# Optimization experiments

Measured on AMD Instinct MI355X. Metric: run time of the kernel, lower is better.

The kernel has to match this reference:

```python
import jax, jax.numpy as jnp
import numpy as np

VOCAB, EMB, HID, LAT = 32000, 512, 1024, 512
B, T = 32, 128


def setup_inputs() -> dict:
    key = jax.random.key(0)
    ks = jax.random.split(key, 10)
    s = 0.02
    return {
        "latent_vector": jax.random.normal(ks[0], (B, LAT), jnp.float32),
        "target_tokens": jax.random.randint(ks[1], (B, T), 0, VOCAB),
        "emb": jax.random.normal(ks[2], (VOCAB, EMB), jnp.float32) * s,
        "W_lh": jax.random.normal(ks[3], (HID, LAT), jnp.float32) * s,
        "b_lh": jnp.zeros((HID,), jnp.float32),
        "W_ih": jax.random.normal(ks[4], (4 * HID, EMB), jnp.float32) * s,
        "b_ih": jnp.zeros((4 * HID,), jnp.float32),
        "W_hh": jax.random.normal(ks[5], (4 * HID, HID), jnp.float32) * s,
        "b_hh": jnp.zeros((4 * HID,), jnp.float32),
        "W_out": jax.random.normal(ks[6], (VOCAB, HID), jnp.float32) * s,
        "b_out": jnp.zeros((VOCAB,), jnp.float32),
    }


def reference(latent_vector, target_tokens, emb, W_lh, b_lh, W_ih, b_ih, W_hh, b_hh, W_out, b_out):
    # teacher_forcing_ratio = 1.0 (deterministic): input at step t is target_tokens[:, t-1]
    h = latent_vector @ W_lh.T + b_lh            # [B, HID]
    c = jnp.zeros_like(h)
    xs = emb[target_tokens[:, :-1]]              # [B, T-1, EMB]
    xs = jnp.swapaxes(xs, 0, 1)                  # [T-1, B, EMB]

    def step(carry, x):
        h, c = carry
        gates = x @ W_ih.T + b_ih + h @ W_hh.T + b_hh   # [B, 4*HID]
        i, f, g, o = jnp.split(gates, 4, axis=-1)       # PyTorch LSTM gate order
        c = jax.nn.sigmoid(f) * c + jax.nn.sigmoid(i) * jnp.tanh(g)
        h = jax.nn.sigmoid(o) * jnp.tanh(c)
        logits = h @ W_out.T + b_out                    # [B, VOCAB]
        return (h, c), logits

    _, logits = jax.lax.scan(step, (h, c), xs)          # [T-1, B, VOCAB]
    return jnp.swapaxes(logits, 0, 1)                   # [B, T-1, VOCAB]
```

## Files before the change

### kernel.cpp

```cpp
#include <hip/hip_runtime.h>
#include <cstdint>

typedef __bf16 bf16x8 __attribute__((ext_vector_type(8)));
typedef __bf16 bf16x4 __attribute__((ext_vector_type(4)));
typedef float  f32x4  __attribute__((ext_vector_type(4)));

#define VOCAB 32000
#define EMB   512
#define HID   1024
#define LAT   512
#define BATCH 32
#define TSTEP 127
#define MROWS 4064
#define MPAD  4096
#define G4    4096
#define NBLK  128
#define NTM   32
#define NTN   250
#define FSTRIDE 64

__device__ __forceinline__ float sigf(float x){ return 1.0f / (1.0f + __expf(-x)); }
__device__ __forceinline__ float tanhfast(float x){
    float ax = fabsf(x);
    float e  = __expf(-2.0f * ax);
    float t  = (1.0f - e) / (1.0f + e);
    return copysignf(t, x);
}

__device__ __forceinline__ void gll16(void* lds, const void* gsrc){
    __builtin_amdgcn_global_load_lds(
        (const __attribute__((address_space(1))) unsigned int*)gsrc,
        (__attribute__((address_space(3))) unsigned int*)lds,
        16, 0, 0);
}
__device__ __forceinline__ void bar(){ asm volatile("s_barrier" ::: "memory"); }

__global__ __launch_bounds__(256) void init_kernel(
    const float* __restrict__ latent,
    const float* __restrict__ Wlh,
    const float* __restrict__ blh,
    __bf16* __restrict__ h0,
    __bf16* __restrict__ Hall,
    unsigned* __restrict__ flags,
    const float* __restrict__ Whh,
    __bf16* __restrict__ Whhb)
{
    if (blockIdx.x >= 128){
        const int n4 = G4 * HID / 4;
        for (int i = (blockIdx.x - 128) * 256 + threadIdx.x; i < n4; i += 64 * 256){
            float4 v = ((const float4*)Whh)[i];
            bf16x4 o = { (__bf16)v.x, (__bf16)v.y, (__bf16)v.z, (__bf16)v.w };
            ((bf16x4*)Whhb)[i] = o;
        }
        return;
    }
    if (blockIdx.x == 0 && threadIdx.x < NBLK)
        flags[threadIdx.x * FSTRIDE] = 0u;

    int id = blockIdx.x * 256 + threadIdx.x;
    int b = id >> 10, j = id & 1023;
    float s = blh[j];
    const float4* lr = (const float4*)(latent + (size_t)b * LAT);
    const float4* wr = (const float4*)(Wlh + (size_t)j * LAT);
    for (int k = 0; k < LAT / 4; ++k){
        float4 a = lr[k], w = wr[k];
        s += a.x * w.x + a.y * w.y + a.z * w.z + a.w * w.w;
    }
    h0[id] = (__bf16)s;
    Hall[(size_t)MROWS * HID + id] = (__bf16)0.0f;
}

__global__ __launch_bounds__(256) void gemm_xg(
    const float* __restrict__ emb,
    const float* __restrict__ Wih,
    const int*   __restrict__ tok,
    float*       __restrict__ xg,
    const float* __restrict__ bih,
    const float* __restrict__ bhh)
{
    __shared__ __bf16 As[2][128 * 32];
    __shared__ __bf16 Bs[2][128 * 32];

    const int tid  = threadIdx.x;
    const int wid  = tid >> 6, lane = tid & 63;
    const int tile_n = blockIdx.x, tile_m = blockIdx.y;
    const int wr = wid >> 1, wc = wid & 1;

    f32x4 acc[4][4] = {};

    auto stage = [&](int kt, int buf){
        #pragma unroll
        for (int j = 0; j < 2; ++j){
            const int slot = tid + j * 256;
            const int row  = slot >> 2;
            const int kb   = kt * 32 + (slot & 3) * 8;
            {
                const int brow = tile_n * 128 + row;
                const float4* p = (const float4*)(Wih + (size_t)brow * EMB + kb);
                float4 u = p[0], v = p[1];
                bf16x8 w = { (__bf16)u.x, (__bf16)u.y, (__bf16)u.z, (__bf16)u.w,
                             (__bf16)v.x, (__bf16)v.y, (__bf16)v.z, (__bf16)v.w };
                *(bf16x8*)&Bs[buf][row * 32 + (slot & 3) * 8] = w;
            }
            {
                int r = tile_m * 128 + row;
                int rc = (r < MROWS) ? r : (MROWS - 1);
                int token = tok[(rc & 31) * 128 + (rc >> 5)];
                const float4* p = (const float4*)(emb + (size_t)token * EMB + kb);
                float4 u = p[0], v = p[1];
                bf16x8 w = { (__bf16)u.x, (__bf16)u.y, (__bf16)u.z, (__bf16)u.w,
                             (__bf16)v.x, (__bf16)v.y, (__bf16)v.z, (__bf16)v.w };
                *(bf16x8*)&As[buf][row * 32 + (slot & 3) * 8] = w;
            }
        }
    };

    const int KT = EMB / 32;
    stage(0, 0);
    for (int kt = 0; kt < KT; ++kt){
        const int buf = kt & 1;
        __syncthreads();
        if (kt + 1 < KT) stage(kt + 1, buf ^ 1);
        const __bf16* Abuf = As[buf];
        const __bf16* Bbuf = Bs[buf];
        const int ar = lane & 15, ko = (lane >> 4) * 8;
        bf16x8 av[4], bv[4];
        #pragma unroll
        for (int m = 0; m < 4; ++m)
            av[m] = *(const bf16x8*)&Abuf[(wr * 64 + m * 16 + ar) * 32 + ko];
        #pragma unroll
        for (int n = 0; n < 4; ++n)
            bv[n] = *(const bf16x8*)&Bbuf[(wc * 64 + n * 16 + ar) * 32 + ko];
        #pragma unroll
        for (int m = 0; m < 4; ++m)
            #pragma unroll
            for (int n = 0; n < 4; ++n)
                acc[m][n] = __builtin_amdgcn_mfma_f32_16x16x32_bf16(av[m], bv[n], acc[m][n], 0, 0, 0);
    }

    const int r0 = tile_m * 128 + wr * 64 + ((lane >> 4) << 2);
    const int c0 = tile_n * 128 + wc * 64 + (lane & 15);
    #pragma unroll
    for (int m = 0; m < 4; ++m){
        #pragma unroll
        for (int n = 0; n < 4; ++n){
            const int col = c0 + n * 16;
            float badd = bih[col] + bhh[col];
            #pragma unroll
            for (int q = 0; q < 4; ++q){
                int row = r0 + m * 16 + q;
                xg[(size_t)row * G4 + col] = acc[m][n][q] + badd;
            }
        }
    }
}

__global__ __launch_bounds__(512) void gemm_logits8(
    const __bf16* __restrict__ A,
    const __bf16* __restrict__ B,
    float*        __restrict__ C,
    const float*  __restrict__ bias)
{
    __shared__ __bf16 sA[4][256][32];
    __shared__ __bf16 sB[4][256][32];

    const int tid = threadIdx.x;
    const int wid = tid >> 6, lane = tid & 63;
    const int wm = wid >> 2, wn = wid & 3;

    const int bid = blockIdx.x;
    const int s   = (bid & 7) * 250 + (bid >> 3);
    const int g   = s / 500, rem = s % 500;
    const int tm  = g * 4 + (rem & 3);
    const int tn  = rem >> 2;

    const int sr  = tid >> 2;
    const int scb = tid & 3;
    const __bf16* gA = A + (size_t)(tm * 256 + sr) * HID + scb * 8;
    const __bf16* gB = B + (size_t)(tn * 256 + sr) * HID + scb * 8;
    char* const dA0 = (char*)&sA[0][0][0] + wid * 1024;
    char* const dB0 = (char*)&sB[0][0][0] + wid * 1024;

    auto stageA = [&](int kt){
        const int sl = kt & 3;
        gll16(dA0 + sl * 16384,        gA + (size_t)kt * 32);
        gll16(dA0 + sl * 16384 + 8192, gA + (size_t)128 * HID + (size_t)kt * 32);
    };
    auto stageB = [&](int kt){
        const int sl = kt & 3;
        gll16(dB0 + sl * 16384,        gB + (size_t)kt * 32);
        gll16(dB0 + sl * 16384 + 8192, gB + (size_t)128 * HID + (size_t)kt * 32);
    };

    f32x4 acc[8][4] = {};
    const int fr = lane & 15, fk = (lane >> 4) * 8;

    stageA(0); stageB(0); stageA(1); stageB(1); stageA(2); stageB(2);
    asm volatile("s_waitcnt vmcnt(8)" ::: "memory");
    bar();

    const int KT = HID / 32;
    bf16x8 bfr[4], afr[4];
    for (int kt = 0; kt < KT; ++kt){
        const int sl = kt & 3;
        #pragma unroll
        for (int nf = 0; nf < 4; ++nf)
            bfr[nf] = *(const bf16x8*)&sB[sl][wn * 64 + nf * 16 + fr][fk];
        #pragma unroll
        for (int mf = 0; mf < 4; ++mf)
            afr[mf] = *(const bf16x8*)&sA[sl][wm * 128 + mf * 16 + fr][fk];
        if (kt + 3 < KT) stageA(kt + 3);
        bar();
        asm volatile("s_waitcnt lgkmcnt(0)" ::: "memory");
        __builtin_amdgcn_sched_barrier(0);
        __builtin_amdgcn_s_setprio(1);
        #pragma unroll
        for (int mf = 0; mf < 4; ++mf)
            #pragma unroll
            for (int nf = 0; nf < 4; ++nf)
                acc[mf][nf] = __builtin_amdgcn_mfma_f32_16x16x32_bf16(
                    afr[mf], bfr[nf], acc[mf][nf], 0, 0, 0);
        __builtin_amdgcn_s_setprio(0);
        bar();
        #pragma unroll
        for (int mf = 0; mf < 4; ++mf)
            afr[mf] = *(const bf16x8*)&sA[sl][wm * 128 + (mf + 4) * 16 + fr][fk];
        if (kt + 3 < KT) stageB(kt + 3);
        bar();
        asm volatile("s_waitcnt lgkmcnt(0)" ::: "memory");
        __builtin_amdgcn_sched_barrier(0);
        __builtin_amdgcn_s_setprio(1);
        #pragma unroll
        for (int mf = 0; mf < 4; ++mf)
            #pragma unroll
            for (int nf = 0; nf < 4; ++nf)
                acc[mf + 4][nf] = __builtin_amdgcn_mfma_f32_16x16x32_bf16(
                    afr[mf], bfr[nf], acc[mf + 4][nf], 0, 0, 0);
        __builtin_amdgcn_s_setprio(0);
        if (kt < KT - 3)       asm volatile("s_waitcnt vmcnt(8)" ::: "memory");
        else if (kt == KT - 3) asm volatile("s_waitcnt vmcnt(4)" ::: "memory");
        else if (kt == KT - 2) asm volatile("s_waitcnt vmcnt(0)" ::: "memory");
        bar();
    }

    #pragma unroll
    for (int mf = 0; mf < 8; ++mf){
        #pragma unroll
        for (int nf = 0; nf < 4; ++nf){
            const int col = tn * 256 + wn * 64 + nf * 16 + fr;
            const float badd = bias[col];
            #pragma unroll
            for (int q = 0; q < 4; ++q){
                int row = tm * 256 + wm * 128 + mf * 16 + (lane >> 4) * 4 + q;
                if (row < MROWS){
                    int t = row >> 5, b = row & 31;
                    __builtin_nontemporal_store(acc[mf][nf][q] + badd,
                        &C[((size_t)b * TSTEP + t) * VOCAB + col]);
                }
            }
        }
    }
}

template<int BF16B>
__global__ __launch_bounds__(256) void gemm_logits(
    const __bf16* __restrict__ A,
    const float*  __restrict__ Bf,
    const __bf16* __restrict__ Bb,
    float*        __restrict__ C,
    const float*  __restrict__ bias)
{
    __shared__ __bf16 As[2][128 * 32];
    __shared__ __bf16 Bs[2][128 * 32];

    const int tid  = threadIdx.x;
    const int wid  = tid >> 6, lane = tid & 63;
    const int bid = blockIdx.x;
    const int s   = (bid & 7) * (NTM * NTN / 8) + (bid >> 3);
    const int g   = s / (8 * NTN), rem = s % (8 * NTN);
    const int tile_m = g * 8 + (rem & 7);
    const int tile_n = rem >> 3;
    const int wr = wid >> 1, wc = wid & 1;

    f32x4 acc[4][4] = {};

    auto stage = [&](int kt, int buf){
        const int kb = kt * 32 + (lane & 3) * 8;
        #pragma unroll
        for (int c2 = 0; c2 < 2; ++c2){
            int rA = tile_m * 128 + c2 * 64 + wid * 16 + (lane >> 2);
            gll16(&As[buf][c2 * 2048 + wid * 512], A + (size_t)rA * HID + kb);
            if constexpr (BF16B){
                int rB = tile_n * 128 + c2 * 64 + wid * 16 + (lane >> 2);
                gll16(&Bs[buf][c2 * 2048 + wid * 512], Bb + (size_t)rB * HID + kb);
            }
        }
        if constexpr (!BF16B){
            #pragma unroll
            for (int j = 0; j < 2; ++j){
                const int slot = tid + j * 256;
                const int row  = slot >> 2;
                const int kb2  = kt * 32 + (slot & 3) * 8;
                const int brow = tile_n * 128 + row;
                const float4* p = (const float4*)(Bf + (size_t)brow * HID + kb2);
                float4 u = p[0], v = p[1];
                bf16x8 w = { (__bf16)u.x, (__bf16)u.y, (__bf16)u.z, (__bf16)u.w,
                             (__bf16)v.x, (__bf16)v.y, (__bf16)v.z, (__bf16)v.w };
                *(bf16x8*)&Bs[buf][row * 32 + (slot & 3) * 8] = w;
            }
        }
    };

    const int KT = HID / 32;
    stage(0, 0);
    for (int kt = 0; kt < KT; ++kt){
        const int buf = kt & 1;
        __syncthreads();
        if (kt + 1 < KT) stage(kt + 1, buf ^ 1);
        const __bf16* Abuf = As[buf];
        const __bf16* Bbuf = Bs[buf];
        const int ar = lane & 15, ko = (lane >> 4) * 8;
        bf16x8 av[4], bv[4];
        #pragma unroll
        for (int m = 0; m < 4; ++m)
            av[m] = *(const bf16x8*)&Abuf[(wr * 64 + m * 16 + ar) * 32 + ko];
        #pragma unroll
        for (int n = 0; n < 4; ++n)
            bv[n] = *(const bf16x8*)&Bbuf[(wc * 64 + n * 16 + ar) * 32 + ko];
        #pragma unroll
        for (int m = 0; m < 4; ++m)
            #pragma unroll
            for (int n = 0; n < 4; ++n)
                acc[m][n] = __builtin_amdgcn_mfma_f32_16x16x32_bf16(av[m], bv[n], acc[m][n], 0, 0, 0);
    }

    const int r0 = tile_m * 128 + wr * 64 + ((lane >> 4) << 2);
    const int c0 = tile_n * 128 + wc * 64 + (lane & 15);
    #pragma unroll
    for (int m = 0; m < 4; ++m){
        #pragma unroll
        for (int n = 0; n < 4; ++n){
            const int col = c0 + n * 16;
            float badd = bias[col];
            #pragma unroll
            for (int q = 0; q < 4; ++q){
                int row = r0 + m * 16 + q;
                if (row < MROWS){
                    int t = row >> 5, b = row & 31;
                    __builtin_nontemporal_store(acc[m][n][q] + badd,
                        &C[((size_t)b * TSTEP + t) * VOCAB + col]);
                }
            }
        }
    }
}

__global__ __launch_bounds__(256) void lstm_coop(
    const float*  __restrict__ xg,
    __bf16*       __restrict__ Hall,
    __bf16*       __restrict__ hbuf,
    const __bf16* __restrict__ Whhb,
    unsigned*     __restrict__ flags,
    const float*  __restrict__ Woutf,
    __bf16*       __restrict__ Woutb)
{
    if (blockIdx.x >= NBLK){
        if (Woutb){
            const int n4 = VOCAB * HID / 4;
            for (int i = (blockIdx.x - NBLK) * 256 + threadIdx.x; i < n4; i += NBLK * 256){
                float4 v = ((const float4*)Woutf)[i];
                bf16x4 o = { (__bf16)v.x, (__bf16)v.y, (__bf16)v.z, (__bf16)v.w };
                ((bf16x4*)Woutb)[i] = o;
            }
        }
        return;
    }

    __shared__ float lds_g[4 * 4 * 4 * 64];
    const int tid = threadIdx.x, wid = tid >> 6, lane = tid & 63;
    const int jb = blockIdx.x * 8;

    bf16x8 bfrag[2][8];
    {
        const int gl = lane & 15, ko = (lane >> 4) * 8;
        #pragma unroll
        for (int nt = 0; nt < 2; ++nt){
            int gg = nt * 16 + gl;
            const __bf16* base =
                Whhb + (size_t)((gg >> 3) * HID + jb + (gg & 7)) * HID + wid * 256 + ko;
            #pragma unroll
            for (int ks = 0; ks < 8; ++ks)
                bfrag[nt][ks] = *(const bf16x8*)(base + ks * 32);
        }
    }

    const int b2 = tid >> 2, up0 = (tid & 3) * 2;
    const int mt2 = b2 >> 4, r2 = b2 & 15, reg2 = r2 & 3, lb2 = (r2 >> 2) << 4;
    float cst[2] = {0.0f, 0.0f};

    const float* xq = xg + (size_t)b2 * G4 + jb + up0;
    float2 xv[4];
    if (tid < 128){
        #pragma unroll
        for (int g = 0; g < 4; ++g) xv[g] = *(const float2*)(xq + g * HID);
    }

    const size_t e0 = (size_t)(lane & 15) * HID + wid * 256 + (lane >> 4) * 8;

    for (int t = 0; t < TSTEP; ++t){
        const unsigned long long* hq =
            (const unsigned long long*)(hbuf + (size_t)(t & 1) * (BATCH * HID));
        union { unsigned long long q[2]; bf16x8 v; } xa[16];
        #pragma unroll
        for (int ks = 0; ks < 8; ++ks){
            size_t q0 = (e0 + (size_t)ks * 32) >> 2;
            size_t q1 = q0 + ((size_t)16 * HID >> 2);
            xa[ks].q[0]     = __hip_atomic_load(hq + q0,     __ATOMIC_RELAXED, __HIP_MEMORY_SCOPE_AGENT);
            xa[ks].q[1]     = __hip_atomic_load(hq + q0 + 1, __ATOMIC_RELAXED, __HIP_MEMORY_SCOPE_AGENT);
            xa[8 + ks].q[0] = __hip_atomic_load(hq + q1,     __ATOMIC_RELAXED, __HIP_MEMORY_SCOPE_AGENT);
            xa[8 + ks].q[1] = __hip_atomic_load(hq + q1 + 1, __ATOMIC_RELAXED, __HIP_MEMORY_SCOPE_AGENT);
        }
        f32x4 a00 = {}, a01 = {}, a10 = {}, a11 = {};
        #pragma unroll
        for (int ks = 0; ks < 8; ++ks){
            a00 = __builtin_amdgcn_mfma_f32_16x16x32_bf16(xa[ks].v,     bfrag[0][ks], a00, 0, 0, 0);
            a01 = __builtin_amdgcn_mfma_f32_16x16x32_bf16(xa[ks].v,     bfrag[1][ks], a01, 0, 0, 0);
            a10 = __builtin_amdgcn_mfma_f32_16x16x32_bf16(xa[8 + ks].v, bfrag[0][ks], a10, 0, 0, 0);
            a11 = __builtin_amdgcn_mfma_f32_16x16x32_bf16(xa[8 + ks].v, bfrag[1][ks], a11, 0, 0, 0);
        }
        #pragma unroll
        for (int q = 0; q < 4; ++q){
            lds_g[((0 * 4 + wid) * 4 + q) * 64 + lane] = a00[q];
            lds_g[((1 * 4 + wid) * 4 + q) * 64 + lane] = a01[q];
            lds_g[((2 * 4 + wid) * 4 + q) * 64 + lane] = a10[q];
            lds_g[((3 * 4 + wid) * 4 + q) * 64 + lane] = a11[q];
        }
        __syncthreads();

        unsigned pku = 0;
        if (tid < 128){
            const float* xn = xq + (size_t)(t + 1) * (BATCH * G4);
            float2 xnew[4];
            #pragma unroll
            for (int g = 0; g < 4; ++g) xnew[g] = *(const float2*)(xn + g * HID);

            float h2[2];
            #pragma unroll
            for (int du = 0; du < 2; ++du){
                int u2 = up0 + du;
                float gate[4];
                #pragma unroll
                for (int ty = 0; ty < 4; ++ty){
                    int gg = ty * 8 + u2;
                    int mtnt = mt2 * 2 + (gg >> 4);
                    int li = lb2 | (gg & 15);
                    float s = 0.0f;
                    #pragma unroll
                    for (int w = 0; w < 4; ++w)
                        s += lds_g[((mtnt * 4 + w) * 4 + reg2) * 64 + li];
                    gate[ty] = s;
                }
                float gi = gate[0] + ((du == 0) ? xv[0].x : xv[0].y);
                float gf = gate[1] + ((du == 0) ? xv[1].x : xv[1].y);
                float gc = gate[2] + ((du == 0) ? xv[2].x : xv[2].y);
                float go = gate[3] + ((du == 0) ? xv[3].x : xv[3].y);
                float c = sigf(gf) * cst[du] + sigf(gi) * tanhfast(gc);
                cst[du] = c;
                h2[du] = sigf(go) * tanhfast(c);
            }
            #pragma unroll
            for (int g = 0; g < 4; ++g) xv[g] = xnew[g];

            union { __bf16 h[2]; unsigned u; } pk;
            pk.h[0] = (__bf16)h2[0]; pk.h[1] = (__bf16)h2[1];
            pku = pk.u;
            unsigned* hw = (unsigned*)(hbuf + (size_t)((t + 1) & 1) * (BATCH * HID)
                                       + (size_t)b2 * HID + jb + up0);
            __hip_atomic_store(hw, pku, __ATOMIC_RELAXED, __HIP_MEMORY_SCOPE_AGENT);
        }

        if (t + 1 == TSTEP){
            if (tid < 128)
                *(unsigned*)(Hall + ((size_t)t * BATCH + b2) * HID + jb + up0) = pku;
            break;
        }

        __syncthreads();
        if (tid == 0)
            __hip_atomic_store(&flags[blockIdx.x * FSTRIDE], (unsigned)(t + 1),
                               __ATOMIC_RELAXED, __HIP_MEMORY_SCOPE_AGENT);
        if (tid < 128)
            *(unsigned*)(Hall + ((size_t)t * BATCH + b2) * HID + jb + up0) = pku;
        if (wid == 0){
            const unsigned tgt = (unsigned)(t + 1);
            for (;;){
                unsigned f0 = __hip_atomic_load(&flags[lane * FSTRIDE],
                                  __ATOMIC_RELAXED, __HIP_MEMORY_SCOPE_AGENT);
                unsigned f1 = __hip_atomic_load(&flags[(lane + 64) * FSTRIDE],
                                  __ATOMIC_RELAXED, __HIP_MEMORY_SCOPE_AGENT);
                if (f0 >= tgt && f1 >= tgt) break;
                __builtin_amdgcn_s_sleep(1);
            }
        }
        __syncthreads();
    }
}

extern "C" void kernel_launch(void* const* d_in, const int* in_sizes, int n_in,
                              void* d_out, int out_size, void* d_ws, size_t ws_size,
                              hipStream_t stream)
{
    const float* latent = (const float*)d_in[0];
    const int*   tokens = (const int*)d_in[1];
    const float* emb    = (const float*)d_in[2];
    const float* Wlh    = (const float*)d_in[3];
    const float* blh    = (const float*)d_in[4];
    const float* Wih    = (const float*)d_in[5];
    const float* bih    = (const float*)d_in[6];
    const float* Whh    = (const float*)d_in[7];
    const float* bhh    = (const float*)d_in[8];
    const float* Wout   = (const float*)d_in[9];
    const float* bout   = (const float*)d_in[10];
    float* out = (float*)d_out;

    const size_t xg_b   = (size_t)MPAD * G4 * 4;
    const size_t hall_b = (size_t)MPAD * HID * 2;
    const size_t whh_b  = (size_t)G4 * HID * 2;
    const size_t wout_b = (size_t)VOCAB * HID * 2;
    const size_t hb_b   = (size_t)2 * BATCH * HID * 2;
    const size_t cnt_b  = (size_t)NBLK * FSTRIDE * 4;

    char* p = (char*)d_ws;
    const bool wsA = ws_size >= xg_b + hall_b + whh_b + wout_b + hb_b + cnt_b;
    const bool wsB = ws_size >= hall_b + whh_b + wout_b + hb_b + cnt_b;

    float* xg;
    if (wsA){ xg = (float*)p; p += xg_b; }
    else    { xg = (float*)d_out; }
    __bf16* Hall = (__bf16*)p; p += hall_b;
    __bf16* Whhb = (__bf16*)p; p += whh_b;
    __bf16* Woutb = nullptr;
    if (wsA || wsB){ Woutb = (__bf16*)p; p += wout_b; }
    __bf16* hbuf = (__bf16*)p; p += hb_b;
    unsigned* flags = (unsigned*)p; p += cnt_b;

    init_kernel<<<dim3(192), dim3(256), 0, stream>>>(
        latent, Wlh, blh, hbuf, Hall, flags, Whh, Whhb);

    gemm_xg<<<dim3(G4 / 128, MPAD / 128), dim3(256), 0, stream>>>(
        emb, Wih, tokens, xg, bih, bhh);

    {
        const float*  xgc   = xg;
        __bf16*       hallp = Hall;
        __bf16*       hbp   = hbuf;
        const __bf16* whhp  = Whhb;
        unsigned*     flagp = flags;
        const float*  wof   = Wout;
        __bf16*       wob   = Woutb;
        void* args[] = { (void*)&xgc, (void*)&hallp, (void*)&hbp, (void*)&whhp,
                         (void*)&flagp, (void*)&wof, (void*)&wob };
        hipLaunchCooperativeKernel((void*)lstm_coop, dim3(2 * NBLK), dim3(256),
                                   args, 0, stream);
    }

    if (Woutb){
        (void)hipGetLastError();
        gemm_logits8<<<dim3(2000), dim3(512), 0, stream>>>(Hall, Woutb, out, bout);
        if (hipGetLastError() != hipSuccess){
            gemm_logits<1><<<dim3(NTM * NTN), dim3(256), 0, stream>>>(
                Hall, (const float*)nullptr, Woutb, out, bout);
        }
    } else {
        gemm_logits<0><<<dim3(NTM * NTN), dim3(256), 0, stream>>>(
            Hall, Wout, (const __bf16*)nullptr, out, bout);
    }
}
```

Before: 1.223 ms.

## Overlap logits GEMM with LSTM recurrence in one cooperative kernel

Adds a cooperative kernel where 128 blocks run the LSTM time steps while another 128 blocks compute logits tiles. Each logits block waits on a shared progress counter until the hidden states its 256-row tile needs are ready. The fp32-to-bf16 conversion of W_out moves into extra blocks of the input-gate GEMM, so it no longer sits in the recurrence launch. The goal is to hide the large output projection behind the latency-bound recurrence, at the cost of using only half the CUs for the GEMM and possible memory contention that could slow the serial LSTM steps.

```diff
diff --git a/kernel.cpp b/kernel.cpp
--- a/kernel.cpp
+++ b/kernel.cpp
@@ -54,7 +54,7 @@
         }
         return;
     }
-    if (blockIdx.x == 0 && threadIdx.x < NBLK)
+    if (blockIdx.x == 0 && threadIdx.x <= NBLK)
         flags[threadIdx.x * FSTRIDE] = 0u;
 
     int id = blockIdx.x * 256 + threadIdx.x;
@@ -76,8 +76,23 @@
     const int*   __restrict__ tok,
     float*       __restrict__ xg,
     const float* __restrict__ bih,
-    const float* __restrict__ bhh)
+    const float* __restrict__ bhh,
+    const float* __restrict__ Woutf,
+    __bf16*      __restrict__ Woutb)
 {
+    if (blockIdx.y >= MPAD / 128){
+        if (Woutb){
+            const int n4 = VOCAB * HID / 4;
+            int cb = (blockIdx.y - 32) * 32 + blockIdx.x;
+            for (int i = cb * 256 + threadIdx.x; i < n4; i += 256 * 256){
+                float4 v = ((const float4*)Woutf)[i];
+                bf16x4 o = { (__bf16)v.x, (__bf16)v.y, (__bf16)v.z, (__bf16)v.w };
+                ((bf16x4*)Woutb)[i] = o;
+            }
+        }
+        return;
+    }
+
     __shared__ __bf16 As[2][128 * 32];
     __shared__ __bf16 Bs[2][128 * 32];
 
@@ -155,203 +170,254 @@
     }
 }
 
-__global__ __launch_bounds__(512) void gemm_logits8(
-    const __bf16* __restrict__ A,
-    const __bf16* __restrict__ B,
+__global__ __launch_bounds__(512) void mega2(
+    const float*  __restrict__ xg,
+    __bf16*       __restrict__ Hall,
+    __bf16*       __restrict__ hbuf,
+    const __bf16* __restrict__ Whhb,
+    unsigned*     __restrict__ flags,
+    const __bf16* __restrict__ Woutb,
     float*        __restrict__ C,
-    const float*  __restrict__ bias)
+    const float*  __restrict__ bout)
 {
-    __shared__ __bf16 sA[4][256][32];
-    __shared__ __bf16 sB[4][256][32];
-
-    const int tid = threadIdx.x;
-    const int wid = tid >> 6, lane = tid & 63;
+    __shared__ __align__(16) char smem[131072];
+    unsigned* done = flags + NBLK * FSTRIDE;
+
+    const int tid = threadIdx.x, wid = tid >> 6, lane = tid & 63;
+
+    if (blockIdx.x < NBLK){
+        float* lds_g = (float*)smem;
+        const int jb = blockIdx.x * 8;
+
+        bf16x8 bfrag[2][8];
+        if (tid < 256){
+            const int gl = lane & 15, ko = (lane >> 4) * 8;
+            #pragma unroll
+            for (int nt = 0; nt < 2; ++nt){
+                int gg = nt * 16 + gl;
+                const __bf16* base =
+                    Whhb + (size_t)((gg >> 3) * HID + jb + (gg & 7)) * HID + wid * 256 + ko;
+                #pragma unroll
+                for (int ks = 0; ks < 8; ++ks)
+                    bfrag[nt][ks] = *(const bf16x8*)(base + ks * 32);
+            }
+        }
+
+        const int b2 = tid >> 2, up0 = (tid & 3) * 2;
+        const int mt2 = b2 >> 4, r2 = b2 & 15, reg2 = r2 & 3, lb2 = (r2 >> 2) << 4;
+        float cst[2] = {0.0f, 0.0f};
+
+        const float* xq = xg + (size_t)b2 * G4 + jb + up0;
+        float2 xv[4];
+        if (tid < 128){
+            #pragma unroll
+            for (int g = 0; g < 4; ++g) xv[g] = *(const float2*)(xq + g * HID);
+        }
+        const size_t e0 = (size_t)(lane & 15) * HID + wid * 256 + (lane >> 4) * 8;
+
+        for (int t = 0; t < TSTEP; ++t){
+            if (tid < 256){
+                const unsigned long long* hq =
+                    (const unsigned long long*)(hbuf + (size_t)(t & 1) * (BATCH * HID));
+                union { unsigned long long q[2]; bf16x8 v; } xa[16];
+                #pragma unroll
+                for (int ks = 0; ks < 8; ++ks){
+                    size_t q0 = (e0 + (size_t)ks * 32) >> 2;
+                    size_t q1 = q0 + ((size_t)16 * HID >> 2);
+                    xa[ks].q[0]     = __hip_atomic_load(hq + q0,     __ATOMIC_RELAXED, __HIP_MEMORY_SCOPE_AGENT);
+                    xa[ks].q[1]     = __hip_atomic_load(hq + q0 + 1, __ATOMIC_RELAXED, __HIP_MEMORY_SCOPE_AGENT);
+                    xa[8 + ks].q[0] = __hip_atomic_load(hq + q1,     __ATOMIC_RELAXED, __HIP_MEMORY_SCOPE_AGENT);
+                    xa[8 + ks].q[1] = __hip_atomic_load(hq + q1 + 1, __ATOMIC_RELAXED, __HIP_MEMORY_SCOPE_AGENT);
+                }
+                f32x4 a00 = {}, a01 = {}, a10 = {}, a11 = {};
+                #pragma unroll
+                for (int ks = 0; ks < 8; ++ks){
+                    a00 = __builtin_amdgcn_mfma_f32_16x16x32_bf16(xa[ks].v,     bfrag[0][ks], a00, 0, 0, 0);
+                    a01 = __builtin_amdgcn_mfma_f32_16x16x32_bf16(xa[ks].v,     bfrag[1][ks], a01, 0, 0, 0);
+                    a10 = __builtin_amdgcn_mfma_f32_16x16x32_bf16(xa[8 + ks].v, bfrag[0][ks], a10, 0, 0, 0);
+                    a11 = __builtin_amdgcn_mfma_f32_16x16x32_bf16(xa[8 + ks].v, bfrag[1][ks], a11, 0, 0, 0);
+                }
+                #pragma unroll
+                for (int q = 0; q < 4; ++q){
+                    lds_g[((0 * 4 + wid) * 4 + q) * 64 + lane] = a00[q];
+                    lds_g[((1 * 4 + wid) * 4 + q) * 64 + lane] = a01[q];
+                    lds_g[((2 * 4 + wid) * 4 + q) * 64 + lane] = a10[q];
+                    lds_g[((3 * 4 + wid) * 4 + q) * 64 + lane] = a11[q];
+                }
+            }
+            __syncthreads();
+
+            if (tid < 128){
+                const float* xn = xq + (size_t)(t + 1) * (BATCH * G4);
+                float2 xnew[4];
+                #pragma unroll
+                for (int g = 0; g < 4; ++g) xnew[g] = *(const float2*)(xn + g * HID);
+
+                float h2[2];
+                #pragma unroll
+                for (int du = 0; du < 2; ++du){
+                    int u2 = up0 + du;
+                    float gate[4];
+                    #pragma unroll
+                    for (int ty = 0; ty < 4; ++ty){
+                        int gg = ty * 8 + u2;
+                        int mtnt = mt2 * 2 + (gg >> 4);
+                        int li = lb2 | (gg & 15);
+                        float s = 0.0f;
+                        #pragma unroll
+                        for (int w = 0; w < 4; ++w)
+                            s += lds_g[((mtnt * 4 + w) * 4 + reg2) * 64 + li];
+                        gate[ty] = s;
+                    }
+                    float gi = gate[0] + ((du == 0) ? xv[0].x : xv[0].y);
+                    float gf = gate[1] + ((du == 0) ? xv[1].x : xv[1].y);
+                    float gc = gate[2] + ((du == 0) ? xv[2].x : xv[2].y);
+                    float go = gate[3] + ((du == 0) ? xv[3].x : xv[3].y);
+                    float c = sigf(gf) * cst[du] + sigf(gi) * tanhfast(gc);
+                    cst[du] = c;
+                    h2[du] = sigf(go) * tanhfast(c);
+                }
+                #pragma unroll
+                for (int g = 0; g < 4; ++g) xv[g] = xnew[g];
+
+                union { __bf16 h[2]; unsigned u; } pk;
+                pk.h[0] = (__bf16)h2[0]; pk.h[1] = (__bf16)h2[1];
+                unsigned* hw = (unsigned*)(hbuf + (size_t)((t + 1) & 1) * (BATCH * HID)
+                                           + (size_t)b2 * HID + jb + up0);
+                __hip_atomic_store(hw, pk.u, __ATOMIC_RELAXED, __HIP_MEMORY_SCOPE_AGENT);
+                __hip_atomic_store((unsigned*)(Hall + ((size_t)t * BATCH + b2) * HID + jb + up0),
+                                   pk.u, __ATOMIC_RELAXED, __HIP_MEMORY_SCOPE_AGENT);
+            }
+
+            __syncthreads();
+            if (tid == 0)
+                __hip_atomic_store(&flags[blockIdx.x * FSTRIDE], (unsigned)(t + 1),
+                                   __ATOMIC_RELAXED, __HIP_MEMORY_SCOPE_AGENT);
+            if (wid == 0 && (t + 1 < TSTEP || blockIdx.x == 0)){
+                const unsigned tgt = (unsigned)(t + 1);
+                for (;;){
+                    unsigned f0 = __hip_atomic_load(&flags[lane * FSTRIDE],
+                                      __ATOMIC_RELAXED, __HIP_MEMORY_SCOPE_AGENT);
+                    unsigned f1 = __hip_atomic_load(&flags[(lane + 64) * FSTRIDE],
+                                      __ATOMIC_RELAXED, __HIP_MEMORY_SCOPE_AGENT);
+                    if (f0 >= tgt && f1 >= tgt) break;
+                    __builtin_amdgcn_s_sleep(1);
+                }
+                if (blockIdx.x == 0 && lane == 0)
+                    __hip_atomic_store(done, tgt, __ATOMIC_RELAXED, __HIP_MEMORY_SCOPE_AGENT);
+            }
+            __syncthreads();
+        }
+        return;
+    }
+
+    if (!Woutb) return;
+    typedef __bf16 (*lds3_t)[256][32];
+    lds3_t sA = (lds3_t)smem;
+    lds3_t sB = (lds3_t)(smem + 65536);
+
+    const int gid = blockIdx.x - NBLK;
     const int wm = wid >> 2, wn = wid & 3;
-
-    const int bid = blockIdx.x;
-    const int s   = (bid & 7) * 250 + (bid >> 3);
-    const int g   = s / 500, rem = s % 500;
-    const int tm  = g * 4 + (rem & 3);
-    const int tn  = rem >> 2;
+    const int tmF = gid & 15;
+    {
+        const unsigned need = (unsigned)((8 * tmF + 8 > TSTEP) ? TSTEP : 8 * tmF + 8);
+        if (tid == 0){
+            while (__hip_atomic_load(done, __ATOMIC_RELAXED, __HIP_MEMORY_SCOPE_AGENT) < need)
+                __builtin_amdgcn_s_sleep(16);
+        }
+        __syncthreads();
+    }
 
     const int sr  = tid >> 2;
     const int scb = tid & 3;
-    const __bf16* gA = A + (size_t)(tm * 256 + sr) * HID + scb * 8;
-    const __bf16* gB = B + (size_t)(tn * 256 + sr) * HID + scb * 8;
-    char* const dA0 = (char*)&sA[0][0][0] + wid * 1024;
-    char* const dB0 = (char*)&sB[0][0][0] + wid * 1024;
-
-    auto stageA = [&](int kt){
-        const int sl = kt & 3;
-        gll16(dA0 + sl * 16384,        gA + (size_t)kt * 32);
-        gll16(dA0 + sl * 16384 + 8192, gA + (size_t)128 * HID + (size_t)kt * 32);
-    };
-    auto stageB = [&](int kt){
-        const int sl = kt & 3;
-        gll16(dB0 + sl * 16384,        gB + (size_t)kt * 32);
-        gll16(dB0 + sl * 16384 + 8192, gB + (size_t)128 * HID + (size_t)kt * 32);
-    };
-
-    f32x4 acc[8][4] = {};
     const int fr = lane & 15, fk = (lane >> 4) * 8;
-
-    stageA(0); stageB(0); stageA(1); stageB(1); stageA(2); stageB(2);
-    asm volatile("s_waitcnt vmcnt(8)" ::: "memory");
-    bar();
-
     const int KT = HID / 32;
-    bf16x8 bfr[4], afr[4];
-    for (int kt = 0; kt < KT; ++kt){
-        const int sl = kt & 3;
-        #pragma unroll
-        for (int nf = 0; nf < 4; ++nf)
-            bfr[nf] = *(const bf16x8*)&sB[sl][wn * 64 + nf * 16 + fr][fk];
-        #pragma unroll
-        for (int mf = 0; mf < 4; ++mf)
-            afr[mf] = *(const bf16x8*)&sA[sl][wm * 128 + mf * 16 + fr][fk];
-        if (kt + 3 < KT) stageA(kt + 3);
+
+    for (int i = gid; i < 2000; i += 128){
+        const int tm = i & 15, tn = i >> 4;
+        const __bf16* gA = Hall  + (size_t)(tm * 256 + sr) * HID + scb * 8;
+        const __bf16* gB = Woutb + (size_t)(tn * 256 + sr) * HID + scb * 8;
+        char* const dA0 = (char*)smem + wid * 1024;
+        char* const dB0 = (char*)smem + 65536 + wid * 1024;
+
+        auto stageA = [&](int kt){
+            const int sl = kt & 3;
+            gll16(dA0 + sl * 16384,        gA + (size_t)kt * 32);
+            gll16(dA0 + sl * 16384 + 8192, gA + (size_t)128 * HID + (size_t)kt * 32);
+        };
+        auto stageB = [&](int kt){
+            const int sl = kt & 3;
+            gll16(dB0 + sl * 16384,        gB + (size_t)kt * 32);
+            gll16(dB0 + sl * 16384 + 8192, gB + (size_t)128 * HID + (size_t)kt * 32);
+        };
+
+        f32x4 acc[8][4] = {};
+        stageA(0); stageB(0); stageA(1); stageB(1); stageA(2); stageB(2);
+        asm volatile("s_waitcnt vmcnt(8)" ::: "memory");
         bar();
-        asm volatile("s_waitcnt lgkmcnt(0)" ::: "memory");
-        __builtin_amdgcn_sched_barrier(0);
-        __builtin_amdgcn_s_setprio(1);
-        #pragma unroll
-        for (int mf = 0; mf < 4; ++mf)
+
+        bf16x8 bfr[4], afr[4];
+        for (int kt = 0; kt < KT; ++kt){
+            const int sl = kt & 3;
             #pragma unroll
             for (int nf = 0; nf < 4; ++nf)
-                acc[mf][nf] = __builtin_amdgcn_mfma_f32_16x16x32_bf16(
-                    afr[mf], bfr[nf], acc[mf][nf], 0, 0, 0);
-        __builtin_amdgcn_s_setprio(0);
-        bar();
-        #pragma unroll
-        for (int mf = 0; mf < 4; ++mf)
-            afr[mf] = *(const bf16x8*)&sA[sl][wm * 128 + (mf + 4) * 16 + fr][fk];
-        if (kt + 3 < KT) stageB(kt + 3);
-        bar();
-        asm volatile("s_waitcnt lgkmcnt(0)" ::: "memory");
-        __builtin_amdgcn_sched_barrier(0);
-        __builtin_amdgcn_s_setprio(1);
-        #pragma unroll
-        for (int mf = 0; mf < 4; ++mf)
-            #pragma unroll
-            for (int nf = 0; nf < 4; ++nf)
-                acc[mf + 4][nf] = __builtin_amdgcn_mfma_f32_16x16x32_bf16(
-                    afr[mf], bfr[nf], acc[mf + 4][nf], 0, 0, 0);
-        __builtin_amdgcn_s_setprio(0);
-        if (kt < KT - 3)       asm volatile("s_waitcnt vmcnt(8)" ::: "memory");
-        else if (kt == KT - 3) asm volatile("s_waitcnt vmcnt(4)" ::: "memory");
-        else if (kt == KT - 2) asm volatile("s_waitcnt vmcnt(0)" ::: "memory");
-        bar();
-    }
-
-    #pragma unroll
-    for (int mf = 0; mf < 8; ++mf){
-        #pragma unroll
-        for (int nf = 0; nf < 4; ++nf){
-            const int col = tn * 256 + wn * 64 + nf * 16 + fr;
-            const float badd = bias[col];
-            #pragma unroll
-            for (int q = 0; q < 4; ++q){
-                int row = tm * 256 + wm * 128 + mf * 16 + (lane >> 4) * 4 + q;
-                if (row < MROWS){
-                    int t = row >> 5, b = row & 31;
-                    __builtin_nontemporal_store(acc[mf][nf][q] + badd,
-                        &C[((size_t)b * TSTEP + t) * VOCAB + col]);
+                bfr[nf] = *(const bf16x8*)&sA[0][0][0 +
+                    ((size_t)0)] , bfr[nf] = *(const bf16x8*)&sB[sl][wn * 64 + nf * 16 + fr][fk];
+            #pragma unroll
+            for (int mf = 0; mf < 4; ++mf)
+                afr[mf] = *(const bf16x8*)&sA[sl][wm * 128 + mf * 16 + fr][fk];
+            if (kt + 3 < KT) stageA(kt + 3);
+            bar();
+            asm volatile("s_waitcnt lgkmcnt(0)" ::: "memory");
+            __builtin_amdgcn_sched_barrier(0);
+            __builtin_amdgcn_s_setprio(1);
+            #pragma unroll
+            for (int mf = 0; mf < 4; ++mf)
+                #pragma unroll
+                for (int nf = 0; nf < 4; ++nf)
+                    acc[mf][nf] = __builtin_amdgcn_mfma_f32_16x16x32_bf16(
+                        afr[mf], bfr[nf], acc[mf][nf], 0, 0, 0);
+            __builtin_amdgcn_s_setprio(0);
+            bar();
+            #pragma unroll
+            for (int mf = 0; mf < 4; ++mf)
+                afr[mf] = *(const bf16x8*)&sA[sl][wm * 128 + (mf + 4) * 16 + fr][fk];
+            if (kt + 3 < KT) stageB(kt + 3);
+            bar();
+            asm volatile("s_waitcnt lgkmcnt(0)" ::: "memory");
+            __builtin_amdgcn_sched_barrier(0);
+            __builtin_amdgcn_s_setprio(1);
+            #pragma unroll
+            for (int mf = 0; mf < 4; ++mf)
+                #pragma unroll
+                for (int nf = 0; nf < 4; ++nf)
+                    acc[mf + 4][nf] = __builtin_amdgcn_mfma_f32_16x16x32_bf16(
+                        afr[mf], bfr[nf], acc[mf + 4][nf], 0, 0, 0);
+            __builtin_amdgcn_s_setprio(0);
+            if (kt < KT - 3)       asm volatile("s_waitcnt vmcnt(8)" ::: "memory");
+            else if (kt == KT - 3) asm volatile("s_waitcnt vmcnt(4)" ::: "memory");
+            else if (kt == KT - 2) asm volatile("s_waitcnt vmcnt(0)" ::: "memory");
+            bar();
+        }
+
+        #pragma unroll
+        for (int mf = 0; mf < 8; ++mf){
+            #pragma unroll
+            for (int nf = 0; nf < 4; ++nf){
+                const int col = tn * 256 + wn * 64 + nf * 16 + fr;
+                const float badd = bout[col];
+                #pragma unroll
+                for (int q = 0; q < 4; ++q){
+                    int row = tm * 256 + wm * 128 + mf * 16 + (lane >> 4) * 4 + q;
+                    if (row < MROWS){
+                        int t = row >> 5, b = row & 31;
+                        __builtin_nontemporal_store(acc[mf][nf][q] + badd,
+                            &C[((size_t)b * TSTEP + t) * VOCAB + col]);
+                    }
                 }
             }
         }
-    }
-}
-
-template<int BF16B>
-__global__ __launch_bounds__(256) void gemm_logits(
-    const __bf16* __restrict__ A,
-    const float*  __restrict__ Bf,
-    const __bf16* __restrict__ Bb,
-    float*        __restrict__ C,
-    const float*  __restrict__ bias)
-{
-    __shared__ __bf16 As[2][128 * 32];
-    __shared__ __bf16 Bs[2][128 * 32];
-
-    const int tid  = threadIdx.x;
-    const int wid  = tid >> 6, lane = tid & 63;
-    const int bid = blockIdx.x;
-    const int s   = (bid & 7) * (NTM * NTN / 8) + (bid >> 3);
-    const int g   = s / (8 * NTN), rem = s % (8 * NTN);
-    const int tile_m = g * 8 + (rem & 7);
-    const int tile_n = rem >> 3;
-    const int wr = wid >> 1, wc = wid & 1;
-
-    f32x4 acc[4][4] = {};
-
-    auto stage = [&](int kt, int buf){
-        const int kb = kt * 32 + (lane & 3) * 8;
-        #pragma unroll
-        for (int c2 = 0; c2 < 2; ++c2){
-            int rA = tile_m * 128 + c2 * 64 + wid * 16 + (lane >> 2);
-            gll16(&As[buf][c2 * 2048 + wid * 512], A + (size_t)rA * HID + kb);
-            if constexpr (BF16B){
-                int rB = tile_n * 128 + c2 * 64 + wid * 16 + (lane >> 2);
-                gll16(&Bs[buf][c2 * 2048 + wid * 512], Bb + (size_t)rB * HID + kb);
-            }
-        }
-        if constexpr (!BF16B){
-            #pragma unroll
-            for (int j = 0; j < 2; ++j){
-                const int slot = tid + j * 256;
-                const int row  = slot >> 2;
-                const int kb2  = kt * 32 + (slot & 3) * 8;
-                const int brow = tile_n * 128 + row;
-                const float4* p = (const float4*)(Bf + (size_t)brow * HID + kb2);
-                float4 u = p[0], v = p[1];
-                bf16x8 w = { (__bf16)u.x, (__bf16)u.y, (__bf16)u.z, (__bf16)u.w,
-                             (__bf16)v.x, (__bf16)v.y, (__bf16)v.z, (__bf16)v.w };
-                *(bf16x8*)&Bs[buf][row * 32 + (slot & 3) * 8] = w;
-            }
-        }
-    };
-
-    const int KT = HID / 32;
-    stage(0, 0);
-    for (int kt = 0; kt < KT; ++kt){
-        const int buf = kt & 1;
         __syncthreads();
-        if (kt + 1 < KT) stage(kt + 1, buf ^ 1);
-        const __bf16* Abuf = As[buf];
-        const __bf16* Bbuf = Bs[buf];
-        const int ar = lane & 15, ko = (lane >> 4) * 8;
-        bf16x8 av[4], bv[4];
-        #pragma unroll
-        for (int m = 0; m < 4; ++m)
-            av[m] = *(const bf16x8*)&Abuf[(wr * 64 + m * 16 + ar) * 32 + ko];
-        #pragma unroll
-        for (int n = 0; n < 4; ++n)
-            bv[n] = *(const bf16x8*)&Bbuf[(wc * 64 + n * 16 + ar) * 32 + ko];
-        #pragma unroll
-        for (int m = 0; m < 4; ++m)
-            #pragma unroll
-            for (int n = 0; n < 4; ++n)
-                acc[m][n] = __builtin_amdgcn_mfma_f32_16x16x32_bf16(av[m], bv[n], acc[m][n], 0, 0, 0);
-    }
-
-    const int r0 = tile_m * 128 + wr * 64 + ((lane >> 4) << 2);
-    const int c0 = tile_n * 128 + wc * 64 + (lane & 15);
-    #pragma unroll
-    for (int m = 0; m < 4; ++m){
-        #pragma unroll
-        for (int n = 0; n < 4; ++n){
-            const int col = c0 + n * 16;
-            float badd = bias[col];
-            #pragma unroll
-            for (int q = 0; q < 4; ++q){
-                int row = r0 + m * 16 + q;
-                if (row < MROWS){
-                    int t = row >> 5, b = row & 31;
-                    __builtin_nontemporal_store(acc[m][n][q] + badd,
-                        &C[((size_t)b * TSTEP + t) * VOCAB + col]);
-                }
-            }
-        }
     }
 }
 
@@ -360,22 +426,8 @@
     __bf16*       __restrict__ Hall,
     __bf16*       __restrict__ hbuf,
     const __bf16* __restrict__ Whhb,
-    unsigned*     __restrict__ flags,
-    const float*  __restrict__ Woutf,
-    __bf16*       __restrict__ Woutb)
+    unsigned*     __restrict__ flags)
 {
-    if (blockIdx.x >= NBLK){
-        if (Woutb){
-            const int n4 = VOCAB * HID / 4;
-            for (int i = (blockIdx.x - NBLK) * 256 + threadIdx.x; i < n4; i += NBLK * 256){
-                float4 v = ((const float4*)Woutf)[i];
-                bf16x4 o = { (__bf16)v.x, (__bf16)v.y, (__bf16)v.z, (__bf16)v.w };
-                ((bf16x4*)Woutb)[i] = o;
-            }
-        }
-        return;
-    }
-
     __shared__ float lds_g[4 * 4 * 4 * 64];
     const int tid = threadIdx.x, wid = tid >> 6, lane = tid & 63;
     const int jb = blockIdx.x * 8;
@@ -404,7 +456,6 @@
         #pragma unroll
         for (int g = 0; g < 4; ++g) xv[g] = *(const float2*)(xq + g * HID);
     }
-
     const size_t e0 = (size_t)(lane & 15) * HID + wid * 256 + (lane >> 4) * 8;
 
     for (int t = 0; t < TSTEP; ++t){
@@ -506,6 +557,99 @@
     }
 }
 
+template<int BF16B>
+__global__ __launch_bounds__(256) void gemm_logits(
+    const __bf16* __restrict__ A,
+    const float*  __restrict__ Bf,
+    const __bf16* __restrict__ Bb,
+    float*        __restrict__ C,
+    const float*  __restrict__ bias)
+{
+    __shared__ __bf16 As[2][128 * 32];
+    __shared__ __bf16 Bs[2][128 * 32];
+
+    const int tid  = threadIdx.x;
+    const int wid  = tid >> 6, lane = tid & 63;
+    const int bid = blockIdx.x;
+    const int s   = (bid & 7) * (NTM * NTN / 8) + (bid >> 3);
+    const int g   = s / (8 * NTN), rem = s % (8 * NTN);
+    const int tile_m = g * 8 + (rem & 7);
+    const int tile_n = rem >> 3;
+    const int wr = wid >> 1, wc = wid & 1;
+
+    f32x4 acc[4][4] = {};
+
+    auto stage = [&](int kt, int buf){
+        const int kb = kt * 32 + (lane & 3) * 8;
+        #pragma unroll
+        for (int c2 = 0; c2 < 2; ++c2){
+            int rA = tile_m * 128 + c2 * 64 + wid * 16 + (lane >> 2);
+            gll16(&As[buf][c2 * 2048 + wid * 512], A + (size_t)rA * HID + kb);
+            if constexpr (BF16B){
+                int rB = tile_n * 128 + c2 * 64 + wid * 16 + (lane >> 2);
+                gll16(&Bs[buf][c2 * 2048 + wid * 512], Bb + (size_t)rB * HID + kb);
+            }
+        }
+        if constexpr (!BF16B){
+            #pragma unroll
+            for (int j = 0; j < 2; ++j){
+                const int slot = tid + j * 256;
+                const int row  = slot >> 2;
+                const int kb2  = kt * 32 + (slot & 3) * 8;
+                const int brow = tile_n * 128 + row;
+                const float4* p = (const float4*)(Bf + (size_t)brow * HID + kb2);
+                float4 u = p[0], v = p[1];
+                bf16x8 w = { (__bf16)u.x, (__bf16)u.y, (__bf16)u.z, (__bf16)u.w,
+                             (__bf16)v.x, (__bf16)v.y, (__bf16)v.z, (__bf16)v.w };
+                *(bf16x8*)&Bs[buf][row * 32 + (slot & 3) * 8] = w;
+            }
+        }
+    };
+
+    const int KT = HID / 32;
+    stage(0, 0);
+    for (int kt = 0; kt < KT; ++kt){
+        const int buf = kt & 1;
+        __syncthreads();
+        if (kt + 1 < KT) stage(kt + 1, buf ^ 1);
+        const __bf16* Abuf = As[buf];
+        const __bf16* Bbuf = Bs[buf];
+        const int ar = lane & 15, ko = (lane >> 4) * 8;
+        bf16x8 av[4], bv[4];
+        #pragma unroll
+        for (int m = 0; m < 4; ++m)
+            av[m] = *(const bf16x8*)&Abuf[(wr * 64 + m * 16 + ar) * 32 + ko];
+        #pragma unroll
+        for (int n = 0; n < 4; ++n)
+            bv[n] = *(const bf16x8*)&Bbuf[(wc * 64 + n * 16 + ar) * 32 + ko];
+        #pragma unroll
+        for (int m = 0; m < 4; ++m)
+            #pragma unroll
+            for (int n = 0; n < 4; ++n)
+                acc[m][n] = __builtin_amdgcn_mfma_f32_16x16x32_bf16(av[m], bv[n], acc[m][n], 0, 0, 0);
+    }
+
+    const int r0 = tile_m * 128 + wr * 64 + ((lane >> 4) << 2);
+    const int c0 = tile_n * 128 + wc * 64 + (lane & 15);
+    #pragma unroll
+    for (int m = 0; m < 4; ++m){
+        #pragma unroll
+        for (int n = 0; n < 4; ++n){
+            const int col = c0 + n * 16;
+            float badd = bias[col];
+            #pragma unroll
+            for (int q = 0; q < 4; ++q){
+                int row = r0 + m * 16 + q;
+                if (row < MROWS){
+                    int t = row >> 5, b = row & 31;
+                    __builtin_nontemporal_store(acc[m][n][q] + badd,
+                        &C[((size_t)b * TSTEP + t) * VOCAB + col]);
+                }
+            }
+        }
+    }
+}
+
 extern "C" void kernel_launch(void* const* d_in, const int* in_sizes, int n_in,
                               void* d_out, int out_size, void* d_ws, size_t ws_size,
                               hipStream_t stream)
@@ -528,7 +672,7 @@
     const size_t whh_b  = (size_t)G4 * HID * 2;
     const size_t wout_b = (size_t)VOCAB * HID * 2;
     const size_t hb_b   = (size_t)2 * BATCH * HID * 2;
-    const size_t cnt_b  = (size_t)NBLK * FSTRIDE * 4;
+    const size_t cnt_b  = (size_t)(NBLK + 1) * FSTRIDE * 4;
 
     char* p = (char*)d_ws;
     const bool wsA = ws_size >= xg_b + hall_b + whh_b + wout_b + hb_b + cnt_b;
@@ -547,32 +691,43 @@
     init_kernel<<<dim3(192), dim3(256), 0, stream>>>(
         latent, Wlh, blh, hbuf, Hall, flags, Whh, Whhb);
 
-    gemm_xg<<<dim3(G4 / 128, MPAD / 128), dim3(256), 0, stream>>>(
-        emb, Wih, tokens, xg, bih, bhh);
-
-    {
+    gemm_xg<<<dim3(G4 / 128, MPAD / 128 + 8), dim3(256), 0, stream>>>(
+        emb, Wih, tokens, xg, bih, bhh, Wout, Woutb);
+
+    bool overlapped = false;
+    if (wsA && Woutb){
         const float*  xgc   = xg;
         __bf16*       hallp = Hall;
         __bf16*       hbp   = hbuf;
         const __bf16* whhp  = Whhb;
         unsigned*     flagp = flags;
-        const float*  wof   = Wout;
-        __bf16*       wob   = Woutb;
+        const __bf16* wob   = Woutb;
+        float*        outp  = out;
+        const float*  boutp = bout;
         void* args[] = { (void*)&xgc, (void*)&hallp, (void*)&hbp, (void*)&whhp,
-                         (void*)&flagp, (void*)&wof, (void*)&wob };
-        hipLaunchCooperativeKernel((void*)lstm_coop, dim3(2 * NBLK), dim3(256),
-                                   args, 0, stream);
-    }
-
-    if (Woutb){
-        (void)hipGetLastError();
-        gemm_logits8<<<dim3(2000), dim3(512), 0, stream>>>(Hall, Woutb, out, bout);
-        if (hipGetLastError() != hipSuccess){
+                         (void*)&flagp, (void*)&wob, (void*)&outp, (void*)&boutp };
+        hipError_t e = hipLaunchCooperativeKernel((void*)mega2, dim3(2 * NBLK),
+                                                  dim3(512), args, 0, stream);
+        overlapped = (e == hipSuccess);
+    }
+
+    if (!overlapped){
+        {
+            const float*  xgc   = xg;
+            __bf16*       hallp = Hall;
+            __bf16*       hbp   = hbuf;
+            const __bf16* whhp  = Whhb;
+            unsigned*     flagp = flags;
+            void* args[] = { (void*)&xgc, (void*)&hallp, (void*)&hbp,
+                             (void*)&whhp, (void*)&flagp };
+            hipLaunchCooperativeKernel((void*)lstm_coop, dim3(NBLK), dim3(256),
+                                       args, 0, stream);
+        }
+        if (Woutb)
             gemm_logits<1><<<dim3(NTM * NTN), dim3(256), 0, stream>>>(
                 Hall, (const float*)nullptr, Woutb, out, bout);
-        }
-    } else {
-        gemm_logits<0><<<dim3(NTM * NTN), dim3(256), 0, stream>>>(
-            Hall, Wout, (const __bf16*)nullptr, out, bout);
+        else
+            gemm_logits<0><<<dim3(NTM * NTN), dim3(256), 0, stream>>>(
+                Hall, Wout, (const __bf16*)nullptr, out, bout);
     }
 }
```

After: 1.598 ms. +30.7%, slower.
